# Performance work log

Hardware: AMD Instinct MI355X
Metric: run time of the kernel (lower is better)

The kernel has to match this reference:

```python
import jax, jax.numpy as jnp
import numpy as np

EMBED = 1024
HEAD = 64

def setup_inputs() -> dict:
    key = jax.random.key(0)
    kx, kk, kq, kv = jax.random.split(key, 4)
    x = jax.random.normal(kx, (8, 2048, EMBED), dtype=jnp.float32)
    s = (1.0 / np.sqrt(EMBED)).astype(np.float32) if isinstance(np.sqrt(EMBED), np.ndarray) else np.float32(1.0 / np.sqrt(EMBED))
    # weights stored as [embed, head] so projection is x @ W (equivalent to torch Linear, no bias)
    Wk = jax.random.normal(kk, (EMBED, HEAD), dtype=jnp.float32) * np.float32(EMBED ** -0.5)
    Wq = jax.random.normal(kq, (EMBED, HEAD), dtype=jnp.float32) * np.float32(EMBED ** -0.5)
    Wv = jax.random.normal(kv, (EMBED, HEAD), dtype=jnp.float32) * np.float32(EMBED ** -0.5)
    return {"x": x, "Wk": Wk, "Wq": Wq, "Wv": Wv}

def reference(x, Wk, Wq, Wv):
    B, S, E = x.shape
    k = jnp.einsum('bse,eh->bsh', x, Wk)
    q = jnp.einsum('bse,eh->bsh', x, Wq)
    v = jnp.einsum('bse,eh->bsh', x, Wv)
    # NOTE: original scales by embedding_dim**-0.5, not head_size**-0.5
    scores = jnp.einsum('bqh,bkh->bqk', q, k) * jnp.asarray(E, x.dtype) ** -0.5
    causal = jnp.tril(jnp.ones((S, S), dtype=bool))
    scores = jnp.where(causal, scores, jnp.asarray(-jnp.inf, x.dtype))
    weights = jax.nn.softmax(scores, axis=-1)
    # dropout is identity in eval / p=0
    return jnp.einsum('bqk,bkh->bqh', weights, v)
```

## Files before the change

### kernel.cpp

```cpp
#include <hip/hip_runtime.h>
#include <hip/hip_bf16.h>

typedef __attribute__((ext_vector_type(4))) float f32x4;
typedef __attribute__((ext_vector_type(4))) short s16x4;
typedef __attribute__((ext_vector_type(8))) short s16x8;
typedef __attribute__((ext_vector_type(4))) unsigned short u16x4;

#define MFMA16(a, b, c) __builtin_amdgcn_mfma_f32_16x16x16bf16_1k((a), (b), (c), 0, 0, 0)
#define LOG2E 1.44269504088896340736f
#define NEG_M_L2E (-8.0f * LOG2E)

static __device__ __forceinline__ short f2bf(float f) {
  union { float f; unsigned u; } v; v.f = f;
  unsigned r = v.u + 0x7fffu + ((v.u >> 16) & 1u);
  return (short)(r >> 16);
}
static __device__ __forceinline__ s16x4 vlo(s16x8 v) { return __builtin_shufflevector(v, v, 0, 1, 2, 3); }
static __device__ __forceinline__ s16x4 vhi(s16x8 v) { return __builtin_shufflevector(v, v, 4, 5, 6, 7); }
static __device__ __forceinline__ s16x8 pack8(f32x4 u, f32x4 v) {
  s16x8 r;
  r[0] = f2bf(u[0]); r[1] = f2bf(u[1]); r[2] = f2bf(u[2]); r[3] = f2bf(u[3]);
  r[4] = f2bf(v[0]); r[5] = f2bf(v[1]); r[6] = f2bf(v[2]); r[7] = f2bf(v[3]);
  return r;
}


__global__ __launch_bounds__(256) void wt_kernel(const float* __restrict__ Wq,
                                                 const float* __restrict__ Wk,
                                                 const float* __restrict__ Wv,
                                                 s16x8* __restrict__ wtf) {
  const int sid = blockIdx.x * 256 + threadIdx.x;
  const int lane = sid & 63;
  const int pj = (sid >> 6) % 6;
  const int ks = (sid >> 6) / 6;
  const int l15 = lane & 15, g = lane >> 4;
  s16x8 o;
#pragma unroll
  for (int e = 0; e < 8; e++) {
    const int jj = 2 * pj + (e >> 2);
    const int kk = ks * 16 + 4 * g + (e & 3);
    const int col = (jj & 3) * 16 + l15;
    const float* W = (jj < 4) ? Wq : (jj < 8 ? Wk : Wv);
    const float scl = (jj < 4) ? 0.03125f : 1.0f;
    o[e] = f2bf(W[kk * 64 + col] * scl);
  }
  wtf[sid] = o;
}

__global__ __launch_bounds__(512) void proj_kernel(const float* __restrict__ x,
                                                   const s16x8* __restrict__ wtf,
                                                   s16x8* __restrict__ qf,
                                                   s16x8* __restrict__ kf,
                                                   s16x8* __restrict__ vf) {
  __shared__ char ldsmem[3][40960];
  const int wid = threadIdx.x >> 6;
  const int lane = threadIdx.x & 63;
  const int l15 = lane & 15, g = lane >> 4;
  const int mt = wid & 3, nh = wid >> 2;
  const int tok0 = blockIdx.x * 64;

  const char* xbytes = (const char*)x;
  const char* wbytes = (const char*)wtf;

  f32x4 acc[6];
#pragma unroll
  for (int i = 0; i < 6; i++) acc[i] = (f32x4){0.f, 0.f, 0.f, 0.f};

#define STAGE(buf, kstep)                                                                \
  {                                                                                      \
    const int ks_ = (kstep);                                                             \
    char* const base_ = ldsmem[buf];                                                     \
    _Pragma("unroll")                                                                    \
    for (int i = 0; i < 2; i++) {                                                        \
      const int gb = wid * 128 + i * 64;                                                 \
      const int tok = (gb >> 4) + g;                                                     \
      const char* src = xbytes + (size_t)(tok0 + tok) * 4096 + ks_ * 256 +               \
                        ((size_t)(l15 ^ (tok & 15))) * 16;                               \
      __builtin_amdgcn_global_load_lds((const unsigned*)src,                             \
                                       (unsigned*)(base_ + gb * 16), 16, 0, 0);          \
    }                                                                                    \
    _Pragma("unroll")                                                                    \
    for (int i = 0; i < 3; i++) {                                                        \
      const int gw = wid * 192 + i * 64;                                                 \
      const char* src = wbytes + ((size_t)ks_ * 1536 + gw + lane) * 16;                  \
      __builtin_amdgcn_global_load_lds((const unsigned*)src,                             \
                                       (unsigned*)(base_ + 16384 + gw * 16), 16, 0, 0);  \
    }                                                                                    \
  }

  STAGE(0, 0);
  STAGE(1, 1);

  int curbuf = 0, stgbuf = 2;
  for (int t = 0; t < 16; t++) {
    if (t + 2 < 16) {
      STAGE(stgbuf, t + 2);
      asm volatile("s_waitcnt vmcnt(10)" ::: "memory");
    } else if (t == 14) {
      asm volatile("s_waitcnt vmcnt(5)" ::: "memory");
    } else {
      asm volatile("s_waitcnt vmcnt(0)" ::: "memory");
    }
    __builtin_amdgcn_s_barrier();
    const char* xb = ldsmem[curbuf];
    const char* wb = xb + 16384;
    const int tok = mt * 16 + l15;
    if (nh == 0) {
#pragma unroll
      for (int ks = 0; ks < 4; ks++) {
        const f32x4 xf = *(const f32x4*)(xb + ((size_t)tok * 16 + (((ks * 4 + g) ^ l15))) * 16);
        s16x4 a;
        a[0] = f2bf(xf[0]); a[1] = f2bf(xf[1]); a[2] = f2bf(xf[2]); a[3] = f2bf(xf[3]);
        const s16x8 w0 = *(const s16x8*)(wb + ((size_t)(ks * 6 + 0) * 64 + lane) * 16);
        const s16x8 w1 = *(const s16x8*)(wb + ((size_t)(ks * 6 + 1) * 64 + lane) * 16);
        const s16x8 w2 = *(const s16x8*)(wb + ((size_t)(ks * 6 + 2) * 64 + lane) * 16);
        acc[0] = MFMA16(vlo(w0), a, acc[0]);
        acc[1] = MFMA16(vhi(w0), a, acc[1]);
        acc[2] = MFMA16(vlo(w1), a, acc[2]);
        acc[3] = MFMA16(vhi(w1), a, acc[3]);
        acc[4] = MFMA16(vlo(w2), a, acc[4]);
        acc[5] = MFMA16(vhi(w2), a, acc[5]);
      }
    } else {
#pragma unroll
      for (int ks = 0; ks < 4; ks++) {
        const f32x4 xf = *(const f32x4*)(xb + ((size_t)tok * 16 + (((ks * 4 + g) ^ l15))) * 16);
        s16x4 a;
        a[0] = f2bf(xf[0]); a[1] = f2bf(xf[1]); a[2] = f2bf(xf[2]); a[3] = f2bf(xf[3]);
        const s16x8 w3 = *(const s16x8*)(wb + ((size_t)(ks * 6 + 3) * 64 + lane) * 16);
        const s16x8 w4 = *(const s16x8*)(wb + ((size_t)(ks * 6 + 4) * 64 + lane) * 16);
        const s16x8 w5 = *(const s16x8*)(wb + ((size_t)(ks * 6 + 5) * 64 + lane) * 16);
        acc[0] = MFMA16(vlo(w3), a, acc[0]);
        acc[1] = MFMA16(vhi(w3), a, acc[1]);
        acc[2] = MFMA16(a, vlo(w4), acc[2]);
        acc[3] = MFMA16(a, vhi(w4), acc[3]);
        acc[4] = MFMA16(a, vlo(w5), acc[4]);
        acc[5] = MFMA16(a, vhi(w5), acc[5]);
      }
    }
    asm volatile("" ::: "memory");
    __builtin_amdgcn_s_barrier();
    curbuf = (curbuf == 2) ? 0 : curbuf + 1;
    stgbuf = (stgbuf == 2) ? 0 : stgbuf + 1;
  }
#undef STAGE

  const int gtile = blockIdx.x * 4 + mt;
  const size_t s0 = (size_t)gtile * 128 + lane;
  if (nh == 0) {
    qf[s0] = pack8(acc[0], acc[1]);
    qf[s0 + 64] = pack8(acc[2], acc[3]);
    kf[s0] = pack8(acc[4], acc[5]);
  } else {
    kf[s0 + 64] = pack8(acc[0], acc[1]);
    vf[s0] = pack8(acc[2], acc[3]);
    vf[s0 + 64] = pack8(acc[4], acc[5]);
  }
}

__global__ __launch_bounds__(256) void attn_kernel(const s16x8* __restrict__ qf,
                                                   const s16x8* __restrict__ kf,
                                                   const s16x8* __restrict__ vf,
                                                   float* __restrict__ out) {
  __shared__ s16x8 stage[4][2][256];
  const int wid = threadIdx.x >> 6;
  const int lane = threadIdx.x & 63;
  const int l15 = lane & 15, g = lane >> 4;
  const int b = blockIdx.x & 7;
  const int t = 127 - (blockIdx.x >> 3);
  const int T = t + 1;
  const int qs = (T + 3) >> 2;
  const int kb = min(wid * qs, T);
  const int ke = min(kb + qs, T);

  const s16x8* qp = qf + (size_t)b * 128 * 128;
  const char* kbytes = (const char*)(kf + (size_t)b * 128 * 128);
  const char* vbytes = (const char*)(vf + (size_t)b * 128 * 128);

  const s16x8 q01 = qp[(size_t)t * 128 + lane];
  const s16x8 q23 = qp[(size_t)t * 128 + 64 + lane];

  f32x4 ot[4];
#pragma unroll
  for (int i = 0; i < 4; i++) ot[i] = (f32x4){0.f, 0.f, 0.f, 0.f};
  float psum = 0.f;

#define AST(buf, tile)                                                                  \
  {                                                                                     \
    const size_t toff = (size_t)(tile) * 2048 + (size_t)lane * 16;                      \
    unsigned* const dst_ = (unsigned*)&stage[wid][buf][0];                              \
    __builtin_amdgcn_global_load_lds((const unsigned*)(kbytes + toff), dst_, 16, 0, 0); \
    __builtin_amdgcn_global_load_lds((const unsigned*)(kbytes + toff + 1024),           \
                                     (unsigned*)((char*)dst_ + 1024), 16, 0, 0);        \
    __builtin_amdgcn_global_load_lds((const unsigned*)(vbytes + toff),                  \
                                     (unsigned*)((char*)dst_ + 2048), 16, 0, 0);        \
    __builtin_amdgcn_global_load_lds((const unsigned*)(vbytes + toff + 1024),           \
                                     (unsigned*)((char*)dst_ + 3072), 16, 0, 0);        \
  }

  if (kb < ke) {
    AST(0, kb);
    int cur = 0;
    for (int tile = kb; tile < ke; ++tile) {
      if (tile + 1 < ke) {
        AST(cur ^ 1, tile + 1);
        asm volatile("s_waitcnt vmcnt(4)" ::: "memory");
      } else {
        asm volatile("s_waitcnt vmcnt(0)" ::: "memory");
      }
      const s16x8* sb = &stage[wid][cur][0];
      const s16x8 kA = sb[lane];
      const s16x8 kB = sb[64 + lane];
      const s16x8 vA = sb[128 + lane];
      const s16x8 vB = sb[192 + lane];
      f32x4 st = (f32x4){0.f, 0.f, 0.f, 0.f};
      st = MFMA16(vlo(kA), vlo(q01), st);
      st = MFMA16(vhi(kA), vhi(q01), st);
      st = MFMA16(vlo(kB), vlo(q23), st);
      st = MFMA16(vhi(kB), vhi(q23), st);
      if (tile == t) {
#pragma unroll
        for (int r = 0; r < 4; r++)
          if (4 * g + r > l15) st[r] = -1e30f;
      }
      s16x4 pf;
#pragma unroll
      for (int r = 0; r < 4; r++) {
        const float p = exp2f(st[r] * LOG2E + NEG_M_L2E);
        psum += p;
        pf[r] = f2bf(p);
      }
      ot[0] = MFMA16(vlo(vA), pf, ot[0]);
      ot[1] = MFMA16(vhi(vA), pf, ot[1]);
      ot[2] = MFMA16(vlo(vB), pf, ot[2]);
      ot[3] = MFMA16(vhi(vB), pf, ot[3]);
      cur ^= 1;
    }
  }
#undef AST

  psum += __shfl_xor(psum, 16);
  psum += __shfl_xor(psum, 32);

  __syncthreads();
  float* const red = (float*)&stage[0][0][0];
  {
    const int base = (wid * 64 + lane) * 17;
#pragma unroll
    for (int dt = 0; dt < 4; dt++)
#pragma unroll
      for (int r = 0; r < 4; r++) red[base + dt * 4 + r] = ot[dt][r];
    red[base + 16] = psum;
  }
  __syncthreads();
  if (wid == 0) {
    float o[16];
#pragma unroll
    for (int j = 0; j < 16; j++) o[j] = 0.f;
    float lt = 0.f;
#pragma unroll
    for (int w = 0; w < 4; w++) {
      const float* src = red + (w * 64 + lane) * 17;
      lt += src[16];
#pragma unroll
      for (int j = 0; j < 16; j++) o[j] += src[j];
    }
    const float inv = 1.0f / lt;
    float* ob = out + (size_t)(b * 128 + t) * 1024 + l15 * 64;
#pragma unroll
    for (int dt = 0; dt < 4; dt++) {
      f32x4 v;
#pragma unroll
      for (int r = 0; r < 4; r++) v[r] = o[dt * 4 + r] * inv;
      *(f32x4*)(ob + dt * 16 + 4 * g) = v;
    }
  }
}

extern "C" void kernel_launch(void* const* d_in, const int* in_sizes, int n_in,
                              void* d_out, int out_size, void* d_ws, size_t ws_size,
                              hipStream_t stream) {
  const float* x = (const float*)d_in[0];
  const float* Wk = (const float*)d_in[1];
  const float* Wq = (const float*)d_in[2];
  const float* Wv = (const float*)d_in[3];
  float* out = (float*)d_out;

  char* ws = (char*)d_ws;
  s16x8* wtf = (s16x8*)ws;
  s16x8* qfb = (s16x8*)(ws + 393216);
  s16x8* kfb = (s16x8*)(ws + 2490368);
  s16x8* vfb = (s16x8*)(ws + 4587520);

  wt_kernel<<<96, 256, 0, stream>>>(Wq, Wk, Wv, wtf);
  proj_kernel<<<256, 512, 0, stream>>>(x, wtf, qfb, kfb, vfb);
  attn_kernel<<<1024, 256, 0, stream>>>(qfb, kfb, vfb, out);
}
```

Before: 45.14 us.

## Fuse weight conversion into projection kernel, dropping separate wt_kernel launch

Removes the standalone kernel that converted and scaled the fp32 weights to bf16 fragment layout. Instead, each projection block loads fp32 weights into registers one k-step ahead, scales and packs them, and writes them to LDS inside the pipelined loop, while x keeps its async LDS staging. This saves one kernel launch and the workspace round trip, at the cost of every block redoing the weight conversion and adding register pressure and waitcnt complexity to the pipeline.

Result: no change. 45.68 us (+1.2%).

```diff
diff --git a/kernel.cpp b/kernel.cpp
--- a/kernel.cpp
+++ b/kernel.cpp
@@ -25,30 +25,10 @@
 }
 
 
-__global__ __launch_bounds__(256) void wt_kernel(const float* __restrict__ Wq,
-                                                 const float* __restrict__ Wk,
-                                                 const float* __restrict__ Wv,
-                                                 s16x8* __restrict__ wtf) {
-  const int sid = blockIdx.x * 256 + threadIdx.x;
-  const int lane = sid & 63;
-  const int pj = (sid >> 6) % 6;
-  const int ks = (sid >> 6) / 6;
-  const int l15 = lane & 15, g = lane >> 4;
-  s16x8 o;
-#pragma unroll
-  for (int e = 0; e < 8; e++) {
-    const int jj = 2 * pj + (e >> 2);
-    const int kk = ks * 16 + 4 * g + (e & 3);
-    const int col = (jj & 3) * 16 + l15;
-    const float* W = (jj < 4) ? Wq : (jj < 8 ? Wk : Wv);
-    const float scl = (jj < 4) ? 0.03125f : 1.0f;
-    o[e] = f2bf(W[kk * 64 + col] * scl);
-  }
-  wtf[sid] = o;
-}
-
 __global__ __launch_bounds__(512) void proj_kernel(const float* __restrict__ x,
-                                                   const s16x8* __restrict__ wtf,
+                                                   const float* __restrict__ Wq,
+                                                   const float* __restrict__ Wk,
+                                                   const float* __restrict__ Wv,
                                                    s16x8* __restrict__ qf,
                                                    s16x8* __restrict__ kf,
                                                    s16x8* __restrict__ vf) {
@@ -60,13 +40,27 @@
   const int tok0 = blockIdx.x * 64;
 
   const char* xbytes = (const char*)x;
-  const char* wbytes = (const char*)wtf;
+
+  const float* wbase[3];
+  float wscl[3];
+  int vo[3];
+  int ldso[3];
+#pragma unroll
+  for (int i = 0; i < 3; i++) {
+    const int pr = wid * 3 + i;
+    const int ksS = pr / 6, pS = pr % 6;
+    wbase[i] = (pS < 2) ? Wq : (pS < 4 ? Wk : Wv);
+    wscl[i] = (pS < 2) ? 0.03125f : 1.0f;
+    const int col = ((2 * pS) & 3) * 16 + l15;
+    vo[i] = (ksS * 16 + 4 * g) * 64 + col;
+    ldso[i] = ((ksS * 6 + pS) * 64 + lane) * 16;
+  }
 
   f32x4 acc[6];
 #pragma unroll
   for (int i = 0; i < 6; i++) acc[i] = (f32x4){0.f, 0.f, 0.f, 0.f};
 
-#define STAGE(buf, kstep)                                                                \
+#define XSTG(buf, kstep)                                                                 \
   {                                                                                      \
     const int ks_ = (kstep);                                                             \
     char* const base_ = ldsmem[buf];                                                     \
@@ -79,71 +73,103 @@
       __builtin_amdgcn_global_load_lds((const unsigned*)src,                             \
                                        (unsigned*)(base_ + gb * 16), 16, 0, 0);          \
     }                                                                                    \
+  }
+
+#define WLOAD(lo, hi)                                                                    \
+  {                                                                                      \
     _Pragma("unroll")                                                                    \
     for (int i = 0; i < 3; i++) {                                                        \
-      const int gw = wid * 192 + i * 64;                                                 \
-      const char* src = wbytes + ((size_t)ks_ * 1536 + gw + lane) * 16;                  \
-      __builtin_amdgcn_global_load_lds((const unsigned*)src,                             \
-                                       (unsigned*)(base_ + 16384 + gw * 16), 16, 0, 0);  \
+      const float* bp = wbase[i] + vo[i];                                                \
+      _Pragma("unroll")                                                                  \
+      for (int e = 0; e < 4; e++) { lo[i][e] = bp[e * 64]; hi[i][e] = bp[16 + e * 64]; } \
+      vo[i] += 4096;                                                                     \
     }                                                                                    \
   }
 
-  STAGE(0, 0);
-  STAGE(1, 1);
-
-  int curbuf = 0, stgbuf = 2;
+#define WWRITE(buf, lo, hi)                                                              \
+  {                                                                                      \
+    char* const wdst_ = ldsmem[buf] + 16384;                                             \
+    _Pragma("unroll")                                                                    \
+    for (int i = 0; i < 3; i++) {                                                        \
+      f32x4 a_ = lo[i] * wscl[i];                                                        \
+      f32x4 b_ = hi[i] * wscl[i];                                                        \
+      *(s16x8*)(wdst_ + ldso[i]) = pack8(a_, b_);                                        \
+    }                                                                                    \
+  }
+
+  {
+    f32x4 wlo[3], whi[3];
+    XSTG(0, 0);
+    XSTG(1, 1);
+    WLOAD(wlo, whi);
+    asm volatile("s_waitcnt vmcnt(0)" ::: "memory");
+    WWRITE(0, wlo, whi);
+    __builtin_amdgcn_s_barrier();
+  }
+
+  int curbuf = 0, wbuf = 1, stgbuf = 2;
   for (int t = 0; t < 16; t++) {
-    if (t + 2 < 16) {
-      STAGE(stgbuf, t + 2);
-      asm volatile("s_waitcnt vmcnt(10)" ::: "memory");
-    } else if (t == 14) {
-      asm volatile("s_waitcnt vmcnt(5)" ::: "memory");
-    } else {
-      asm volatile("s_waitcnt vmcnt(0)" ::: "memory");
-    }
-    __builtin_amdgcn_s_barrier();
-    const char* xb = ldsmem[curbuf];
-    const char* wb = xb + 16384;
-    const int tok = mt * 16 + l15;
-    if (nh == 0) {
-#pragma unroll
-      for (int ks = 0; ks < 4; ks++) {
-        const f32x4 xf = *(const f32x4*)(xb + ((size_t)tok * 16 + (((ks * 4 + g) ^ l15))) * 16);
-        s16x4 a;
-        a[0] = f2bf(xf[0]); a[1] = f2bf(xf[1]); a[2] = f2bf(xf[2]); a[3] = f2bf(xf[3]);
-        const s16x8 w0 = *(const s16x8*)(wb + ((size_t)(ks * 6 + 0) * 64 + lane) * 16);
-        const s16x8 w1 = *(const s16x8*)(wb + ((size_t)(ks * 6 + 1) * 64 + lane) * 16);
-        const s16x8 w2 = *(const s16x8*)(wb + ((size_t)(ks * 6 + 2) * 64 + lane) * 16);
-        acc[0] = MFMA16(vlo(w0), a, acc[0]);
-        acc[1] = MFMA16(vhi(w0), a, acc[1]);
-        acc[2] = MFMA16(vlo(w1), a, acc[2]);
-        acc[3] = MFMA16(vhi(w1), a, acc[3]);
-        acc[4] = MFMA16(vlo(w2), a, acc[4]);
-        acc[5] = MFMA16(vhi(w2), a, acc[5]);
-      }
-    } else {
-#pragma unroll
-      for (int ks = 0; ks < 4; ks++) {
-        const f32x4 xf = *(const f32x4*)(xb + ((size_t)tok * 16 + (((ks * 4 + g) ^ l15))) * 16);
-        s16x4 a;
-        a[0] = f2bf(xf[0]); a[1] = f2bf(xf[1]); a[2] = f2bf(xf[2]); a[3] = f2bf(xf[3]);
-        const s16x8 w3 = *(const s16x8*)(wb + ((size_t)(ks * 6 + 3) * 64 + lane) * 16);
-        const s16x8 w4 = *(const s16x8*)(wb + ((size_t)(ks * 6 + 4) * 64 + lane) * 16);
-        const s16x8 w5 = *(const s16x8*)(wb + ((size_t)(ks * 6 + 5) * 64 + lane) * 16);
-        acc[0] = MFMA16(vlo(w3), a, acc[0]);
-        acc[1] = MFMA16(vhi(w3), a, acc[1]);
-        acc[2] = MFMA16(a, vlo(w4), acc[2]);
-        acc[3] = MFMA16(a, vhi(w4), acc[3]);
-        acc[4] = MFMA16(a, vlo(w5), acc[4]);
-        acc[5] = MFMA16(a, vhi(w5), acc[5]);
-      }
+    f32x4 wlo[3], whi[3];
+    if (t + 1 < 16) WLOAD(wlo, whi);
+    __builtin_amdgcn_sched_barrier(0);
+    if (t + 2 < 16) XSTG(stgbuf, t + 2);
+
+    {
+      const char* xb = ldsmem[curbuf];
+      const char* wb = xb + 16384;
+      const int tok = mt * 16 + l15;
+      if (nh == 0) {
+#pragma unroll
+        for (int ks = 0; ks < 4; ks++) {
+          const f32x4 xf = *(const f32x4*)(xb + ((size_t)tok * 16 + (((ks * 4 + g) ^ l15))) * 16);
+          s16x4 a;
+          a[0] = f2bf(xf[0]); a[1] = f2bf(xf[1]); a[2] = f2bf(xf[2]); a[3] = f2bf(xf[3]);
+          const s16x8 w0 = *(const s16x8*)(wb + ((size_t)(ks * 6 + 0) * 64 + lane) * 16);
+          const s16x8 w1 = *(const s16x8*)(wb + ((size_t)(ks * 6 + 1) * 64 + lane) * 16);
+          const s16x8 w2 = *(const s16x8*)(wb + ((size_t)(ks * 6 + 2) * 64 + lane) * 16);
+          acc[0] = MFMA16(vlo(w0), a, acc[0]);
+          acc[1] = MFMA16(vhi(w0), a, acc[1]);
+          acc[2] = MFMA16(vlo(w1), a, acc[2]);
+          acc[3] = MFMA16(vhi(w1), a, acc[3]);
+          acc[4] = MFMA16(vlo(w2), a, acc[4]);
+          acc[5] = MFMA16(vhi(w2), a, acc[5]);
+        }
+      } else {
+#pragma unroll
+        for (int ks = 0; ks < 4; ks++) {
+          const f32x4 xf = *(const f32x4*)(xb + ((size_t)tok * 16 + (((ks * 4 + g) ^ l15))) * 16);
+          s16x4 a;
+          a[0] = f2bf(xf[0]); a[1] = f2bf(xf[1]); a[2] = f2bf(xf[2]); a[3] = f2bf(xf[3]);
+          const s16x8 w3 = *(const s16x8*)(wb + ((size_t)(ks * 6 + 3) * 64 + lane) * 16);
+          const s16x8 w4 = *(const s16x8*)(wb + ((size_t)(ks * 6 + 4) * 64 + lane) * 16);
+          const s16x8 w5 = *(const s16x8*)(wb + ((size_t)(ks * 6 + 5) * 64 + lane) * 16);
+          acc[0] = MFMA16(vlo(w3), a, acc[0]);
+          acc[1] = MFMA16(vhi(w3), a, acc[1]);
+          acc[2] = MFMA16(a, vlo(w4), acc[2]);
+          acc[3] = MFMA16(a, vhi(w4), acc[3]);
+          acc[4] = MFMA16(a, vlo(w5), acc[4]);
+          acc[5] = MFMA16(a, vhi(w5), acc[5]);
+        }
+      }
+    }
+
+    if (t + 1 < 16) {
+      if (t + 2 < 16) {
+        asm volatile("s_waitcnt vmcnt(2)" ::: "memory");
+      } else {
+        asm volatile("s_waitcnt vmcnt(0)" ::: "memory");
+      }
+      WWRITE(wbuf, wlo, whi);
     }
     asm volatile("" ::: "memory");
     __builtin_amdgcn_s_barrier();
     curbuf = (curbuf == 2) ? 0 : curbuf + 1;
+    wbuf = (wbuf == 2) ? 0 : wbuf + 1;
     stgbuf = (stgbuf == 2) ? 0 : stgbuf + 1;
   }
-#undef STAGE
+#undef XSTG
+#undef WLOAD
+#undef WWRITE
 
   const int gtile = blockIdx.x * 4 + mt;
   const size_t s0 = (size_t)gtile * 128 + lane;
@@ -287,12 +313,10 @@
   float* out = (float*)d_out;
 
   char* ws = (char*)d_ws;
-  s16x8* wtf = (s16x8*)ws;
-  s16x8* qfb = (s16x8*)(ws + 393216);
-  s16x8* kfb = (s16x8*)(ws + 2490368);
-  s16x8* vfb = (s16x8*)(ws + 4587520);
-
-  wt_kernel<<<96, 256, 0, stream>>>(Wq, Wk, Wv, wtf);
-  proj_kernel<<<256, 512, 0, stream>>>(x, wtf, qfb, kfb, vfb);
+  s16x8* qfb = (s16x8*)ws;
+  s16x8* kfb = (s16x8*)(ws + 2097152);
+  s16x8* vfb = (s16x8*)(ws + 4194304);
+
+  proj_kernel<<<256, 512, 0, stream>>>(x, Wq, Wk, Wv, qfb, kfb, vfb);
   attn_kernel<<<1024, 256, 0, stream>>>(qfb, kfb, vfb, out);
 }
```

## Load x directly into registers in projection kernel, halve block tile

Applied to the files above, without the earlier changes.

The projection kernel no longer stages the fp32 x tile through LDS. Each lane loads its own x rows straight into a triple-buffered register array, and only the bf16 weight fragments are staged in LDS. Blocks shrink from 512 to 256 threads and from 64 to 32 tokens, so the grid doubles to 512 blocks and LDS per block drops. In exchange each weight tile is reloaded by twice as many blocks, register pressure rises from holding 12 x vectors, and the vmcnt accounting now has to cover both the direct loads and the LDS loads.

Measured after the change: 52.59 us. 1.17x slower.

```diff
diff --git a/kernel.cpp b/kernel.cpp
--- a/kernel.cpp
+++ b/kernel.cpp
@@ -47,68 +47,65 @@
   wtf[sid] = o;
 }
 
-__global__ __launch_bounds__(512) void proj_kernel(const float* __restrict__ x,
+__global__ __launch_bounds__(256) void proj_kernel(const float* __restrict__ x,
                                                    const s16x8* __restrict__ wtf,
                                                    s16x8* __restrict__ qf,
                                                    s16x8* __restrict__ kf,
                                                    s16x8* __restrict__ vf) {
-  __shared__ char ldsmem[3][40960];
+  __shared__ char ldsmem[3][24576];
   const int wid = threadIdx.x >> 6;
   const int lane = threadIdx.x & 63;
   const int l15 = lane & 15, g = lane >> 4;
-  const int mt = wid & 3, nh = wid >> 2;
-  const int tok0 = blockIdx.x * 64;
-
-  const char* xbytes = (const char*)x;
+  const int mt = wid & 1, nh = wid >> 1;
+  const int tok0 = blockIdx.x * 32;
+
+  const float* xp = x + (size_t)(tok0 + mt * 16 + l15) * 1024 + 4 * g;
   const char* wbytes = (const char*)wtf;
 
   f32x4 acc[6];
 #pragma unroll
   for (int i = 0; i < 6; i++) acc[i] = (f32x4){0.f, 0.f, 0.f, 0.f};
 
-#define STAGE(buf, kstep)                                                                \
+  f32x4 xr[3][4];
+
+#define WSTG(bufi, kstep)                                                                \
   {                                                                                      \
-    const int ks_ = (kstep);                                                             \
-    char* const base_ = ldsmem[buf];                                                     \
     _Pragma("unroll")                                                                    \
-    for (int i = 0; i < 2; i++) {                                                        \
-      const int gb = wid * 128 + i * 64;                                                 \
-      const int tok = (gb >> 4) + g;                                                     \
-      const char* src = xbytes + (size_t)(tok0 + tok) * 4096 + ks_ * 256 +               \
-                        ((size_t)(l15 ^ (tok & 15))) * 16;                               \
+    for (int i = 0; i < 6; i++) {                                                        \
+      const int gw = wid * 384 + i * 64;                                                 \
+      const char* src = wbytes + ((size_t)(kstep) * 1536 + gw + lane) * 16;              \
       __builtin_amdgcn_global_load_lds((const unsigned*)src,                             \
-                                       (unsigned*)(base_ + gb * 16), 16, 0, 0);          \
+                                       (unsigned*)(ldsmem[bufi] + gw * 16), 16, 0, 0);   \
     }                                                                                    \
+  }
+
+#define XLOAD(seti, kstep)                                                               \
+  {                                                                                      \
     _Pragma("unroll")                                                                    \
-    for (int i = 0; i < 3; i++) {                                                        \
-      const int gw = wid * 192 + i * 64;                                                 \
-      const char* src = wbytes + ((size_t)ks_ * 1536 + gw + lane) * 16;                  \
-      __builtin_amdgcn_global_load_lds((const unsigned*)src,                             \
-                                       (unsigned*)(base_ + 16384 + gw * 16), 16, 0, 0);  \
-    }                                                                                    \
-  }
-
-  STAGE(0, 0);
-  STAGE(1, 1);
-
-  int curbuf = 0, stgbuf = 2;
+    for (int ks = 0; ks < 4; ks++)                                                       \
+      xr[seti][ks] = *(const f32x4*)(xp + (kstep) * 64 + ks * 16);                       \
+  }
+
+  WSTG(0, 0); XLOAD(0, 0);
+  WSTG(1, 1); XLOAD(1, 1);
+
+#pragma unroll
   for (int t = 0; t < 16; t++) {
     if (t + 2 < 16) {
-      STAGE(stgbuf, t + 2);
+      WSTG((t + 2) % 3, t + 2);
+      XLOAD((t + 2) % 3, t + 2);
+      asm volatile("s_waitcnt vmcnt(20)" ::: "memory");
+    } else if (t == 14) {
       asm volatile("s_waitcnt vmcnt(10)" ::: "memory");
-    } else if (t == 14) {
-      asm volatile("s_waitcnt vmcnt(5)" ::: "memory");
     } else {
       asm volatile("s_waitcnt vmcnt(0)" ::: "memory");
     }
     __builtin_amdgcn_s_barrier();
-    const char* xb = ldsmem[curbuf];
-    const char* wb = xb + 16384;
-    const int tok = mt * 16 + l15;
+    const char* wb = ldsmem[t % 3];
     if (nh == 0) {
 #pragma unroll
       for (int ks = 0; ks < 4; ks++) {
-        const f32x4 xf = *(const f32x4*)(xb + ((size_t)tok * 16 + (((ks * 4 + g) ^ l15))) * 16);
+        const f32x4 xf = xr[t % 3][ks];
         s16x4 a;
         a[0] = f2bf(xf[0]); a[1] = f2bf(xf[1]); a[2] = f2bf(xf[2]); a[3] = f2bf(xf[3]);
         const s16x8 w0 = *(const s16x8*)(wb + ((size_t)(ks * 6 + 0) * 64 + lane) * 16);
@@ -124,7 +121,7 @@
     } else {
 #pragma unroll
       for (int ks = 0; ks < 4; ks++) {
-        const f32x4 xf = *(const f32x4*)(xb + ((size_t)tok * 16 + (((ks * 4 + g) ^ l15))) * 16);
+        const f32x4 xf = xr[t % 3][ks];
         s16x4 a;
         a[0] = f2bf(xf[0]); a[1] = f2bf(xf[1]); a[2] = f2bf(xf[2]); a[3] = f2bf(xf[3]);
         const s16x8 w3 = *(const s16x8*)(wb + ((size_t)(ks * 6 + 3) * 64 + lane) * 16);
@@ -140,12 +137,11 @@
     }
     asm volatile("" ::: "memory");
     __builtin_amdgcn_s_barrier();
-    curbuf = (curbuf == 2) ? 0 : curbuf + 1;
-    stgbuf = (stgbuf == 2) ? 0 : stgbuf + 1;
-  }
-#undef STAGE
-
-  const int gtile = blockIdx.x * 4 + mt;
+  }
+#undef WSTG
+#undef XLOAD
+
+  const int gtile = blockIdx.x * 2 + mt;
   const size_t s0 = (size_t)gtile * 128 + lane;
   if (nh == 0) {
     qf[s0] = pack8(acc[0], acc[1]);
@@ -293,6 +289,6 @@
   s16x8* vfb = (s16x8*)(ws + 4587520);
 
   wt_kernel<<<96, 256, 0, stream>>>(Wq, Wk, Wv, wtf);
-  proj_kernel<<<256, 512, 0, stream>>>(x, wtf, qfb, kfb, vfb);
+  proj_kernel<<<512, 256, 0, stream>>>(x, wtf, qfb, kfb, vfb);
   attn_kernel<<<1024, 256, 0, stream>>>(qfb, kfb, vfb, out);
 }
```
